# Kernel tuning notes

Measured on AMD Instinct MI355X. Metric: run time of the kernel, lower is better.

Reference implementation:

```python
import jax, jax.numpy as jnp
import numpy as np
from jax import lax

T = 8  # primary_vec_length


def setup_inputs() -> dict:
    key = jax.random.key(0)
    k1, k2, k3 = jax.random.split(key, 3)
    x = jax.random.normal(k1, (32, 256, 64, 64), dtype=jnp.float32)
    # Conv2d weight [out_ch, in_ch, kH, kW], kaiming-ish scale
    W = jax.random.normal(k2, (32, 256, 9, 9), dtype=jnp.float32) * 0.01
    b = jax.random.normal(k3, (32,), dtype=jnp.float32) * 0.01
    return {"x": x, "W": W, "b": b}


def reference(x, W, b):
    B = x.shape[0]
    # Conv2d(kernel=9, stride=2, valid). The original applies this conv T times
    # to identical stacked copies of x; compute it once and broadcast (same math).
    conv = lax.conv_general_dilated(
        x, W, window_strides=(2, 2), padding="VALID",
        dimension_numbers=("NCHW", "OIHW", "NCHW"))
    conv = conv + b[None, :, None, None]            # [B, C, H', W']
    s = jnp.broadcast_to(conv[:, None], (B, T) + conv.shape[1:])  # [B, T, C, H', W']
    # squash along dim=1 (the capsule-vector / time dim)
    sq = jnp.sum(s * s, axis=1, keepdims=True)      # [B, 1, C, H', W']
    scale = sq / (1.0 + sq) / jnp.sqrt(sq + 1e-8)
    squ = s * scale                                  # [B, T, C, H', W']
    squ = squ.reshape(B, T, -1)                      # [B, T, C*H'*W']
    squ = jnp.transpose(squ, (0, 2, 1))[..., None]   # [B, N, T, 1]
    return squ
```

## Files before the change

### kernel.cpp

```cpp
#include <hip/hip_runtime.h>
#include <hip/hip_bf16.h>
#include <stdint.h>

typedef _Float16 f16;
typedef _Float16 f16x8 __attribute__((ext_vector_type(8)));
typedef float f32x16 __attribute__((ext_vector_type(16)));
typedef float f32x4 __attribute__((ext_vector_type(4)));
typedef uint32_t u32x4 __attribute__((ext_vector_type(4)));
typedef uint32_t u32x2 __attribute__((ext_vector_type(2)));

#define MFMA(A, B, C) __builtin_amdgcn_mfma_f32_32x32x16_f16((A), (B), (C), 0, 0, 0)

__global__ __launch_bounds__(256) void nchw_to_nhwc_f16(
    const float* __restrict__ x, f16* __restrict__ xt) {
  __shared__ __align__(16) uint32_t tile[64 * 128];
  const int bh = blockIdx.x;
  const int t = threadIdx.x;
  const float* src = x + (size_t)(bh >> 6) * (256 * 4096) + (bh & 63) * 64;

  const int w4 = t & 15;
  const int cq = t >> 4;
  const int xorv = 4 * (w4 & 7);
#pragma unroll
  for (int it = 0; it < 4; ++it) {
    const int c0 = it * 64 + cq * 4;
    float4 v0 = *(const float4*)(src + (size_t)(c0 + 0) * 4096 + w4 * 4);
    float4 v1 = *(const float4*)(src + (size_t)(c0 + 1) * 4096 + w4 * 4);
    float4 v2 = *(const float4*)(src + (size_t)(c0 + 2) * 4096 + w4 * 4);
    float4 v3 = *(const float4*)(src + (size_t)(c0 + 3) * 4096 + w4 * 4);
    const float* p0 = (const float*)&v0;
    const float* p1 = (const float*)&v1;
    const float* p2 = (const float*)&v2;
    const float* p3 = (const float*)&v3;
    const int u = it * 32 + cq * 2;
#pragma unroll
    for (int jw = 0; jw < 4; ++jw) {
      f16 h0 = (f16)p0[jw], h1 = (f16)p1[jw], h2 = (f16)p2[jw], h3 = (f16)p3[jw];
      uint32_t lo = (uint32_t)__builtin_bit_cast(uint16_t, h0) |
                    ((uint32_t)__builtin_bit_cast(uint16_t, h1) << 16);
      uint32_t hi = (uint32_t)__builtin_bit_cast(uint16_t, h2) |
                    ((uint32_t)__builtin_bit_cast(uint16_t, h3) << 16);
      u32x2 pk = {lo, hi};
      const int w = w4 * 4 + jw;
      *(u32x2*)&tile[w * 128 + (u ^ xorv)] = pk;
    }
  }
  __syncthreads();
  f16* dstb = xt + (size_t)bh * 16384;
#pragma unroll
  for (int it = 0; it < 8; ++it) {
    const int n = it * 256 + t;
    const int w2 = n & 31;
    const int par = (n >> 5) & 1;
    const int g8 = n >> 6;
    const int w = par + 2 * w2;
    const u32x4 v = *(const u32x4*)&tile[w * 128 + ((g8 * 4) ^ (4 * ((w >> 2) & 7)))];
    *(u32x4*)(dstb + n * 8) = v;
  }
}

__global__ __launch_bounds__(256) void pack_w(const float* __restrict__ W,
                                              f16* __restrict__ wt) {
  __shared__ float lds[10368];
  const int t = threadIdx.x;
  const int co = blockIdx.x >> 1;
  const int cih = blockIdx.x & 1;
  const float* src = W + (size_t)(co * 256 + cih * 128) * 81;
  for (int i = t; i < 10368; i += 256) lds[i] = src[i];
  __syncthreads();
  for (int j = t; j < 1296; j += 256) {
    const int kk = j >> 4;
    const int t16 = j & 15;
    const int cicl = t16 >> 2;
    const int sg = t16 & 3;
    const int cin = ((sg >> 1) & 1) * 16 + (sg & 1) * 8;
    f16 tmp[8];
#pragma unroll
    for (int e = 0; e < 8; ++e)
      tmp[e] = (f16)lds[(cicl * 32 + cin + e) * 81 + kk];
    const int cic = cih * 4 + cicl;
    *(f16x8*)&wt[(size_t)(((kk * 8 + cic) * 4 + sg) * 32 + co) * 8] = *(f16x8*)tmp;
  }
}

__global__ __launch_bounds__(256, 3) void conv_direct(
    const f16* __restrict__ xt, const f16* __restrict__ wt,
    float* __restrict__ convp) {
  __shared__ float red[4 * 32 * 33];
  const int tid = threadIdx.x;
  const int lane = tid & 63;
  const int wave = tid >> 6;
  const int m = lane & 31;
  const int hh = lane >> 5;

  const int blk = blockIdx.x;
  const int xcd = blk & 7;
  const int r = blk >> 3;
  const int i4 = r / 28;
  const int rr = r - i4 * 28;
  const int bimg = xcd * 4 + i4;
  const int ohp = rr >> 1;
  const int cih = rr & 1;
  const int cic = cih * 4 + wave;

  const char* xb = (const char*)xt;
  const char* wb = (const char*)wt;

  const char* ab = xb + ((size_t)(bimg * 64 + 4 * ohp) * 32768 +
                         cic * 4096 + hh * 1024 + m * 16);
  const int boff = cic * 2048 + hh * 512 + m * 16;

#define ALOAD(AB, KW, P) \
  (*(const f16x8*)((AB) + (P) * 2048 + ((KW)&1) * 512 + ((KW) >> 1) * 16))
#define BLOAD(KK, S) \
  (*(const f16x8*)(wb + (size_t)(KK) * 16384 + (S) * 1024 + boff))

  f32x16 acc0, acc1;
#pragma unroll
  for (int i = 0; i < 16; ++i) { acc0[i] = 0.f; acc1[i] = 0.f; }

#define SLAB_BODY(T0A, T1A, KKB0, KKB1)                                        \
  {                                                                            \
    f16x8 a0[3], a1[3], b00[3], b01[3], b10[3], b11[3];                        \
    _Pragma("unroll") for (int k = 0; k < 3; ++k) {                            \
      a0[k] = ALOAD(ab, k, 0);                                                 \
      a1[k] = ALOAD(ab, k, 1);                                                 \
      if (T0A) { b00[k] = BLOAD((KKB0) + k, 0); b01[k] = BLOAD((KKB0) + k, 1); } \
      if (T1A) { b10[k] = BLOAD((KKB1) + k, 0); b11[k] = BLOAD((KKB1) + k, 1); } \
    }                                                                          \
    _Pragma("unroll") for (int kw = 0; kw < 9; ++kw) {                         \
      const int sl = kw % 3;                                                   \
      const f16x8 ca0 = a0[sl], ca1 = a1[sl];                                  \
      f16x8 t00, t01, t10, t11;                                                \
      if (T0A) { t00 = b00[sl]; t01 = b01[sl]; }                               \
      if (T1A) { t10 = b10[sl]; t11 = b11[sl]; }                               \
      if (kw + 3 < 9) {                                                        \
        a0[sl] = ALOAD(ab, kw + 3, 0);                                         \
        a1[sl] = ALOAD(ab, kw + 3, 1);                                         \
        if (T0A) { b00[sl] = BLOAD((KKB0) + kw + 3, 0);                        \
                   b01[sl] = BLOAD((KKB0) + kw + 3, 1); }                      \
        if (T1A) { b10[sl] = BLOAD((KKB1) + kw + 3, 0);                        \
                   b11[sl] = BLOAD((KKB1) + kw + 3, 1); }                      \
      }                                                                        \
      if (T0A) { acc0 = MFMA(ca0, t00, acc0); acc0 = MFMA(ca1, t01, acc0); }   \
      if (T1A) { acc1 = MFMA(ca0, t10, acc1); acc1 = MFMA(ca1, t11, acc1); }   \
    }                                                                          \
  }

  for (int j = 0; j < 2; ++j) {
    SLAB_BODY(1, 0, j * 9, 0)
    ab += 32768;
  }
  for (int j = 2; j < 9; ++j) {
    SLAB_BODY(1, 1, j * 9, (j - 2) * 9)
    ab += 32768;
  }
  for (int j = 9; j < 11; ++j) {
    SLAB_BODY(0, 1, 0, (j - 2) * 9)
    ab += 32768;
  }
#undef SLAB_BODY
#undef ALOAD
#undef BLOAD

  const int mm = tid >> 3;
  const int c0 = (tid & 7) * 4;
#pragma unroll
  for (int half = 0; half < 2; ++half) {
    __syncthreads();
#pragma unroll
    for (int rI = 0; rI < 16; ++rI) {
      const int row = (rI & 3) + 8 * (rI >> 2) + 4 * hh;
      red[(wave * 32 + row) * 33 + m] = half ? acc1[rI] : acc0[rI];
    }
    __syncthreads();
    if (mm < 28) {
      float s0 = 0.f, s1 = 0.f, s2 = 0.f, s3 = 0.f;
#pragma unroll
      for (int w = 0; w < 4; ++w) {
        const float* rp = red + (w * 32 + mm) * 33 + c0;
        s0 += rp[0]; s1 += rp[1]; s2 += rp[2]; s3 += rp[3];
      }
      const f32x4 o4 = {s0, s1, s2, s3};
      const int p = bimg * 784 + (2 * ohp + half) * 28 + mm;
      *(f32x4*)&convp[(size_t)cih * 802816 + (size_t)p * 32 + c0] = o4;
    }
  }
}

__global__ __launch_bounds__(256) void epilogue(const float* __restrict__ convp,
                                                const float* __restrict__ bias,
                                                float* __restrict__ out) {
  const int gi = blockIdx.x * 256 + threadIdx.x;
  const int base = gi * 8;
  const int p = gi >> 2;
  const int co0 = (gi & 3) * 8;
  const int bi = p / 784;
  const int pix = p - bi * 784;
  f32x4 v0 = {0.f, 0.f, 0.f, 0.f}, v1 = {0.f, 0.f, 0.f, 0.f};
#pragma unroll
  for (int qq = 0; qq < 2; ++qq) {
    v0 += *(const f32x4*)&convp[(size_t)qq * 802816 + base];
    v1 += *(const f32x4*)&convp[(size_t)qq * 802816 + base + 4];
  }
  float vb[8];
#pragma unroll
  for (int jj = 0; jj < 4; ++jj) {
    vb[jj] = v0[jj] + bias[co0 + jj];
    vb[4 + jj] = v1[jj] + bias[co0 + 4 + jj];
  }
  float* ob = out + (size_t)bi * 200704 + pix * 8;
#pragma unroll
  for (int jj = 0; jj < 8; ++jj) {
    const float vv = vb[jj];
    const float sq = 8.f * vv * vv;
    const float scale = sq / ((1.f + sq) * sqrtf(sq + 1e-8f));
    const float y = vv * scale;
    const f32x4 qv = {y, y, y, y};
    float* o = ob + (size_t)(co0 + jj) * 6272;
    *(f32x4*)o = qv;
    *(f32x4*)(o + 4) = qv;
  }
}

extern "C" void kernel_launch(void* const* d_in, const int* in_sizes, int n_in,
                              void* d_out, int out_size, void* d_ws,
                              size_t ws_size, hipStream_t stream) {
  const float* x = (const float*)d_in[0];
  const float* W = (const float*)d_in[1];
  const float* bias = (const float*)d_in[2];
  float* out = (float*)d_out;

  char* ws = (char*)d_ws;
  f16* xt = (f16*)ws;
  f16* wt = (f16*)(ws + 67108864);
  float* convp = (float*)(ws + 67108864 + 1327104);

  nchw_to_nhwc_f16<<<dim3(2048), dim3(256), 0, stream>>>(x, xt);
  pack_w<<<dim3(64), dim3(256), 0, stream>>>(W, wt);
  conv_direct<<<dim3(896), dim3(256), 0, stream>>>(xt, wt, convp);
  epilogue<<<dim3(392), dim3(256), 0, stream>>>(convp, bias, out);
}
```

Baseline: 296.1 us.

## Stage conv weights into LDS with async global_load_lds double buffering

Each wave used to load the weight fragments for every kernel position straight from global memory into registers. Now the whole block cooperatively stages those fragments into a 32 KB shared-memory double buffer with global_load_lds, fetching the next position's weights while it computes the current one. Input fragments are still loaded from global memory one step ahead. This removes redundant per-wave weight traffic and frees registers, but adds a __syncthreads on every kernel step and more LDS per block, which may limit occupancy.

```diff
diff --git a/kernel.cpp b/kernel.cpp
--- a/kernel.cpp
+++ b/kernel.cpp
@@ -86,7 +86,7 @@
 __global__ __launch_bounds__(256, 3) void conv_direct(
     const f16* __restrict__ xt, const f16* __restrict__ wt,
     float* __restrict__ convp) {
-  __shared__ float red[4 * 32 * 33];
+  __shared__ __align__(16) char smem[32768];
   const int tid = threadIdx.x;
   const int lane = tid & 63;
   const int wave = tid >> 6;
@@ -108,61 +108,83 @@
 
   const char* ab = xb + ((size_t)(bimg * 64 + 4 * ohp) * 32768 +
                          cic * 4096 + hh * 1024 + m * 16);
-  const int boff = cic * 2048 + hh * 512 + m * 16;
+  const size_t cih8192 = (size_t)cih * 8192;
+  const int t16 = tid * 16;
+  char* stg = smem;
+  const int fragoff = wave * 2048 + hh * 512 + m * 16;
+
+#define GLDS(G, L)                                                            \
+  __builtin_amdgcn_global_load_lds(                                           \
+      (const __attribute__((address_space(1))) void*)(G),                     \
+      (__attribute__((address_space(3))) void*)(L), 16, 0, 0)
 
 #define ALOAD(AB, KW, P) \
-  (*(const f16x8*)((AB) + (P) * 2048 + ((KW)&1) * 512 + ((KW) >> 1) * 16))
-#define BLOAD(KK, S) \
-  (*(const f16x8*)(wb + (size_t)(KK) * 16384 + (S) * 1024 + boff))
+  (*(const f16x8*)((AB) + (P)*2048 + ((KW)&1) * 512 + ((KW) >> 1) * 16))
+
+#define STAGE(DST, KKA, KKB)                                                  \
+  {                                                                           \
+    const char* sA = wb + (size_t)(KKA)*16384 + cih8192 + t16;                \
+    const char* sB = wb + (size_t)(KKB)*16384 + cih8192 + t16;                \
+    char* d = (DST) + t16;                                                    \
+    GLDS(sA, d);                                                              \
+    GLDS(sA + 4096, d + 4096);                                                \
+    GLDS(sB, d + 8192);                                                       \
+    GLDS(sB + 4096, d + 12288);                                               \
+  }
 
   f32x16 acc0, acc1;
 #pragma unroll
   for (int i = 0; i < 16; ++i) { acc0[i] = 0.f; acc1[i] = 0.f; }
 
-#define SLAB_BODY(T0A, T1A, KKB0, KKB1)                                        \
-  {                                                                            \
-    f16x8 a0[3], a1[3], b00[3], b01[3], b10[3], b11[3];                        \
-    _Pragma("unroll") for (int k = 0; k < 3; ++k) {                            \
-      a0[k] = ALOAD(ab, k, 0);                                                 \
-      a1[k] = ALOAD(ab, k, 1);                                                 \
-      if (T0A) { b00[k] = BLOAD((KKB0) + k, 0); b01[k] = BLOAD((KKB0) + k, 1); } \
-      if (T1A) { b10[k] = BLOAD((KKB1) + k, 0); b11[k] = BLOAD((KKB1) + k, 1); } \
-    }                                                                          \
-    _Pragma("unroll") for (int kw = 0; kw < 9; ++kw) {                         \
-      const int sl = kw % 3;                                                   \
-      const f16x8 ca0 = a0[sl], ca1 = a1[sl];                                  \
-      f16x8 t00, t01, t10, t11;                                                \
-      if (T0A) { t00 = b00[sl]; t01 = b01[sl]; }                               \
-      if (T1A) { t10 = b10[sl]; t11 = b11[sl]; }                               \
-      if (kw + 3 < 9) {                                                        \
-        a0[sl] = ALOAD(ab, kw + 3, 0);                                         \
-        a1[sl] = ALOAD(ab, kw + 3, 1);                                         \
-        if (T0A) { b00[sl] = BLOAD((KKB0) + kw + 3, 0);                        \
-                   b01[sl] = BLOAD((KKB0) + kw + 3, 1); }                      \
-        if (T1A) { b10[sl] = BLOAD((KKB1) + kw + 3, 0);                        \
-                   b11[sl] = BLOAD((KKB1) + kw + 3, 1); }                      \
-      }                                                                        \
-      if (T0A) { acc0 = MFMA(ca0, t00, acc0); acc0 = MFMA(ca1, t01, acc0); }   \
-      if (T1A) { acc1 = MFMA(ca0, t10, acc1); acc1 = MFMA(ca1, t11, acc1); }   \
-    }                                                                          \
-  }
-
-  for (int j = 0; j < 2; ++j) {
-    SLAB_BODY(1, 0, j * 9, 0)
-    ab += 32768;
-  }
-  for (int j = 2; j < 9; ++j) {
-    SLAB_BODY(1, 1, j * 9, (j - 2) * 9)
-    ab += 32768;
-  }
-  for (int j = 9; j < 11; ++j) {
-    SLAB_BODY(0, 1, 0, (j - 2) * 9)
-    ab += 32768;
-  }
-#undef SLAB_BODY
+  STAGE(stg, 0, 0)
+  f16x8 a0n = ALOAD(ab, 0, 0), a1n = ALOAD(ab, 0, 1);
+  int p = 0;
+
+#define STEP(T0A, T1A, NKKA, NKKB, ABN, NKW, LAST)                            \
+  {                                                                           \
+    __syncthreads();                                                          \
+    if (!(LAST)) STAGE(stg + (p ^ 1) * 16384, NKKA, NKKB)                     \
+    const f16x8 ca0 = a0n, ca1 = a1n;                                         \
+    if (!(LAST)) { a0n = ALOAD(ABN, NKW, 0); a1n = ALOAD(ABN, NKW, 1); }      \
+    const char* bp = stg + p * 16384 + fragoff;                               \
+    if (T0A) {                                                                \
+      acc0 = MFMA(ca0, *(const f16x8*)(bp), acc0);                            \
+      acc0 = MFMA(ca1, *(const f16x8*)(bp + 1024), acc0);                     \
+    }                                                                         \
+    if (T1A) {                                                                \
+      acc1 = MFMA(ca0, *(const f16x8*)(bp + 8192), acc1);                     \
+      acc1 = MFMA(ca1, *(const f16x8*)(bp + 9216), acc1);                     \
+    }                                                                         \
+    p ^= 1;                                                                   \
+  }
+
+#define SLAB9(T0A, T1A, KKA0, KKB0, NSA, NSB, ISLAST)                         \
+  {                                                                           \
+    _Pragma("unroll") for (int kw = 0; kw < 9; ++kw) {                        \
+      const int nkka = kw < 8 ? (KKA0) + kw + 1 : (NSA);                      \
+      const int nkkb = kw < 8 ? (KKB0) + kw + 1 : (NSB);                      \
+      const char* abn = kw < 8 ? ab : ab + 32768;                             \
+      const int nkw = kw < 8 ? kw + 1 : 0;                                    \
+      STEP(T0A, T1A, nkka, nkkb, abn, nkw, (ISLAST) && kw == 8)               \
+    }                                                                         \
+    ab += 32768;                                                              \
+  }
+
+  SLAB9(1, 0, 0, 0, 9, 0, 0)
+  SLAB9(1, 0, 9, 0, 18, 0, 0)
+  for (int j = 2; j < 8; ++j) {
+    SLAB9(1, 1, j * 9, (j - 2) * 9, (j + 1) * 9, (j - 1) * 9, 0)
+  }
+  SLAB9(1, 1, 72, 54, 0, 63, 0)
+  SLAB9(0, 1, 0, 63, 0, 72, 0)
+  SLAB9(0, 1, 0, 72, 0, 0, 1)
+#undef SLAB9
+#undef STEP
+#undef STAGE
 #undef ALOAD
-#undef BLOAD
-
+#undef GLDS
+
+  float* red = (float*)smem;
   const int mm = tid >> 3;
   const int c0 = (tid & 7) * 4;
 #pragma unroll
@@ -182,8 +204,8 @@
         s0 += rp[0]; s1 += rp[1]; s2 += rp[2]; s3 += rp[3];
       }
       const f32x4 o4 = {s0, s1, s2, s3};
-      const int p = bimg * 784 + (2 * ohp + half) * 28 + mm;
-      *(f32x4*)&convp[(size_t)cih * 802816 + (size_t)p * 32 + c0] = o4;
+      const int pp = bimg * 784 + (2 * ohp + half) * 28 + mm;
+      *(f32x4*)&convp[(size_t)cih * 802816 + (size_t)pp * 32 + c0] = o4;
     }
   }
 }
```

Result: slower. 376.9 us (+27.3%).

## Compute four output rows per block, reusing weight fragments across rows

Applied to the files above, without the earlier changes.

Each conv block now produces four output rows instead of two, halving the grid. Loops are reordered so kw and kernel-row parity are outer, and each weight fragment loaded once feeds four accumulators. Input rows are shifted through registers in a sliding window. This cuts redundant weight loads per MFMA at the cost of more registers, lower occupancy (launch bound 2) and fewer blocks to spread across CUs.

```diff
diff --git a/kernel.cpp b/kernel.cpp
--- a/kernel.cpp
+++ b/kernel.cpp
@@ -83,7 +83,7 @@
   }
 }
 
-__global__ __launch_bounds__(256, 3) void conv_direct(
+__global__ __launch_bounds__(256, 2) void conv_direct(
     const f16* __restrict__ xt, const f16* __restrict__ wt,
     float* __restrict__ convp) {
   __shared__ float red[4 * 32 * 33];
@@ -96,96 +96,98 @@
   const int blk = blockIdx.x;
   const int xcd = blk & 7;
   const int r = blk >> 3;
-  const int i4 = r / 28;
-  const int rr = r - i4 * 28;
+  const int i4 = r / 14;
+  const int rr = r - i4 * 14;
   const int bimg = xcd * 4 + i4;
-  const int ohp = rr >> 1;
+  const int og = rr >> 1;
   const int cih = rr & 1;
   const int cic = cih * 4 + wave;
 
   const char* xb = (const char*)xt;
   const char* wb = (const char*)wt;
 
-  const char* ab = xb + ((size_t)(bimg * 64 + 4 * ohp) * 32768 +
-                         cic * 4096 + hh * 1024 + m * 16);
+  const char* base = xb + ((size_t)(bimg * 64 + 8 * og) * 32768 +
+                           cic * 4096 + hh * 1024 + m * 16);
   const int boff = cic * 2048 + hh * 512 + m * 16;
 
-#define ALOAD(AB, KW, P) \
-  (*(const f16x8*)((AB) + (P) * 2048 + ((KW)&1) * 512 + ((KW) >> 1) * 16))
-#define BLOAD(KK, S) \
+#define ALOADR(H, KW, P)                                                 \
+  (*(const f16x8*)(base + (size_t)(H) * 32768 + (P) * 2048 +             \
+                   ((KW) & 1) * 512 + ((KW) >> 1) * 16))
+#define BLOADK(KK, S) \
   (*(const f16x8*)(wb + (size_t)(KK) * 16384 + (S) * 1024 + boff))
 
-  f32x16 acc0, acc1;
-#pragma unroll
-  for (int i = 0; i < 16; ++i) { acc0[i] = 0.f; acc1[i] = 0.f; }
-
-#define SLAB_BODY(T0A, T1A, KKB0, KKB1)                                        \
-  {                                                                            \
-    f16x8 a0[3], a1[3], b00[3], b01[3], b10[3], b11[3];                        \
-    _Pragma("unroll") for (int k = 0; k < 3; ++k) {                            \
-      a0[k] = ALOAD(ab, k, 0);                                                 \
-      a1[k] = ALOAD(ab, k, 1);                                                 \
-      if (T0A) { b00[k] = BLOAD((KKB0) + k, 0); b01[k] = BLOAD((KKB0) + k, 1); } \
-      if (T1A) { b10[k] = BLOAD((KKB1) + k, 0); b11[k] = BLOAD((KKB1) + k, 1); } \
-    }                                                                          \
-    _Pragma("unroll") for (int kw = 0; kw < 9; ++kw) {                         \
-      const int sl = kw % 3;                                                   \
-      const f16x8 ca0 = a0[sl], ca1 = a1[sl];                                  \
-      f16x8 t00, t01, t10, t11;                                                \
-      if (T0A) { t00 = b00[sl]; t01 = b01[sl]; }                               \
-      if (T1A) { t10 = b10[sl]; t11 = b11[sl]; }                               \
-      if (kw + 3 < 9) {                                                        \
-        a0[sl] = ALOAD(ab, kw + 3, 0);                                         \
-        a1[sl] = ALOAD(ab, kw + 3, 1);                                         \
-        if (T0A) { b00[sl] = BLOAD((KKB0) + kw + 3, 0);                        \
-                   b01[sl] = BLOAD((KKB0) + kw + 3, 1); }                      \
-        if (T1A) { b10[sl] = BLOAD((KKB1) + kw + 3, 0);                        \
-                   b11[sl] = BLOAD((KKB1) + kw + 3, 1); }                      \
-      }                                                                        \
-      if (T0A) { acc0 = MFMA(ca0, t00, acc0); acc0 = MFMA(ca1, t01, acc0); }   \
-      if (T1A) { acc1 = MFMA(ca0, t10, acc1); acc1 = MFMA(ca1, t11, acc1); }   \
-    }                                                                          \
-  }
-
-  for (int j = 0; j < 2; ++j) {
-    SLAB_BODY(1, 0, j * 9, 0)
-    ab += 32768;
-  }
-  for (int j = 2; j < 9; ++j) {
-    SLAB_BODY(1, 1, j * 9, (j - 2) * 9)
-    ab += 32768;
-  }
-  for (int j = 9; j < 11; ++j) {
-    SLAB_BODY(0, 1, 0, (j - 2) * 9)
-    ab += 32768;
-  }
-#undef SLAB_BODY
-#undef ALOAD
-#undef BLOAD
+  f32x16 acc0, acc1, acc2, acc3;
+#pragma unroll
+  for (int i = 0; i < 16; ++i) {
+    acc0[i] = 0.f; acc1[i] = 0.f; acc2[i] = 0.f; acc3[i] = 0.f;
+  }
+
+#pragma unroll
+  for (int kw = 0; kw < 9; ++kw) {
+#pragma unroll
+    for (int par = 0; par < 2; ++par) {
+      const int nk = par ? 4 : 5;
+      f16x8 bb0[5], bb1[5];
+#pragma unroll
+      for (int i = 0; i < 5; ++i) {
+        if (i < nk) {
+          bb0[i] = BLOADK((par + 2 * i) * 9 + kw, 0);
+          bb1[i] = BLOADK((par + 2 * i) * 9 + kw, 1);
+        }
+      }
+      f16x8 a00 = ALOADR(par + 0, kw, 0), a01 = ALOADR(par + 0, kw, 1);
+      f16x8 a10 = ALOADR(par + 2, kw, 0), a11 = ALOADR(par + 2, kw, 1);
+      f16x8 a20 = ALOADR(par + 4, kw, 0), a21 = ALOADR(par + 4, kw, 1);
+      f16x8 a30 = ALOADR(par + 6, kw, 0), a31 = ALOADR(par + 6, kw, 1);
+#pragma unroll
+      for (int i = 0; i < nk; ++i) {
+        f16x8 n0, n1;
+        if (i + 1 < nk) {
+          n0 = ALOADR(par + 2 * i + 8, kw, 0);
+          n1 = ALOADR(par + 2 * i + 8, kw, 1);
+        }
+        acc0 = MFMA(a00, bb0[i], acc0); acc0 = MFMA(a01, bb1[i], acc0);
+        acc1 = MFMA(a10, bb0[i], acc1); acc1 = MFMA(a11, bb1[i], acc1);
+        acc2 = MFMA(a20, bb0[i], acc2); acc2 = MFMA(a21, bb1[i], acc2);
+        acc3 = MFMA(a30, bb0[i], acc3); acc3 = MFMA(a31, bb1[i], acc3);
+        if (i + 1 < nk) {
+          a00 = a10; a01 = a11;
+          a10 = a20; a11 = a21;
+          a20 = a30; a21 = a31;
+          a30 = n0;  a31 = n1;
+        }
+      }
+    }
+  }
+#undef ALOADR
+#undef BLOADK
 
   const int mm = tid >> 3;
   const int c0 = (tid & 7) * 4;
-#pragma unroll
-  for (int half = 0; half < 2; ++half) {
-    __syncthreads();
-#pragma unroll
-    for (int rI = 0; rI < 16; ++rI) {
-      const int row = (rI & 3) + 8 * (rI >> 2) + 4 * hh;
-      red[(wave * 32 + row) * 33 + m] = half ? acc1[rI] : acc0[rI];
-    }
-    __syncthreads();
-    if (mm < 28) {
-      float s0 = 0.f, s1 = 0.f, s2 = 0.f, s3 = 0.f;
-#pragma unroll
-      for (int w = 0; w < 4; ++w) {
-        const float* rp = red + (w * 32 + mm) * 33 + c0;
-        s0 += rp[0]; s1 += rp[1]; s2 += rp[2]; s3 += rp[3];
-      }
-      const f32x4 o4 = {s0, s1, s2, s3};
-      const int p = bimg * 784 + (2 * ohp + half) * 28 + mm;
-      *(f32x4*)&convp[(size_t)cih * 802816 + (size_t)p * 32 + c0] = o4;
-    }
-  }
+#define REDUCE_ROUND(ACC, T)                                                   \
+  {                                                                            \
+    __syncthreads();                                                           \
+    _Pragma("unroll") for (int rI = 0; rI < 16; ++rI) {                        \
+      const int row = (rI & 3) + 8 * (rI >> 2) + 4 * hh;                       \
+      red[(wave * 32 + row) * 33 + m] = (ACC)[rI];                             \
+    }                                                                          \
+    __syncthreads();                                                           \
+    if (mm < 28) {                                                             \
+      float s0 = 0.f, s1 = 0.f, s2 = 0.f, s3 = 0.f;                            \
+      _Pragma("unroll") for (int w = 0; w < 4; ++w) {                          \
+        const float* rp = red + (w * 32 + mm) * 33 + c0;                       \
+        s0 += rp[0]; s1 += rp[1]; s2 += rp[2]; s3 += rp[3];                    \
+      }                                                                        \
+      const f32x4 o4 = {s0, s1, s2, s3};                                       \
+      const int p = bimg * 784 + (4 * og + (T)) * 28 + mm;                     \
+      *(f32x4*)&convp[(size_t)cih * 802816 + (size_t)p * 32 + c0] = o4;        \
+    }                                                                          \
+  }
+  REDUCE_ROUND(acc0, 0)
+  REDUCE_ROUND(acc1, 1)
+  REDUCE_ROUND(acc2, 2)
+  REDUCE_ROUND(acc3, 3)
+#undef REDUCE_ROUND
 }
 
 __global__ __launch_bounds__(256) void epilogue(const float* __restrict__ convp,
@@ -238,6 +240,6 @@
 
   nchw_to_nhwc_f16<<<dim3(2048), dim3(256), 0, stream>>>(x, xt);
   pack_w<<<dim3(64), dim3(256), 0, stream>>>(W, wt);
-  conv_direct<<<dim3(896), dim3(256), 0, stream>>>(xt, wt, convp);
+  conv_direct<<<dim3(448), dim3(256), 0, stream>>>(xt, wt, convp);
   epilogue<<<dim3(392), dim3(256), 0, stream>>>(convp, bias, out);
 }
```

Result: slower. 312.6 us (+5.6%).

## Share staged weights in LDS across output-row waves, split input channels across blocks

Applied to the files above, without the earlier changes.

Restructures the conv work split so each block owns one input-channel chunk and four waves cover different output row pairs. The weight slab for each kh is staged into a 4-deep LDS ring via global_load_lds and shared by all waves, replacing per-wave direct global weight loads. The cross-wave LDS reduction is removed: each wave writes its partial directly, which grows the partial buffer to 8 channel chunks that the epilogue now sums. The costs are more partial-sum traffic in the epilogue, some idle waves (ohp>=14), lower occupancy, and a barrier per slab.

```diff
diff --git a/kernel.cpp b/kernel.cpp
--- a/kernel.cpp
+++ b/kernel.cpp
@@ -83,10 +83,10 @@
   }
 }
 
-__global__ __launch_bounds__(256, 3) void conv_direct(
+__global__ __launch_bounds__(256, 2) void conv_direct(
     const f16* __restrict__ xt, const f16* __restrict__ wt,
     float* __restrict__ convp) {
-  __shared__ float red[4 * 32 * 33];
+  __shared__ __align__(16) char stg[4 * 18432];
   const int tid = threadIdx.x;
   const int lane = tid & 63;
   const int wave = tid >> 6;
@@ -96,94 +96,102 @@
   const int blk = blockIdx.x;
   const int xcd = blk & 7;
   const int r = blk >> 3;
-  const int i4 = r / 28;
-  const int rr = r - i4 * 28;
+  const int i4 = r >> 5;
+  const int rr = r & 31;
+  const int og = rr >> 3;
+  const int cic = rr & 7;
   const int bimg = xcd * 4 + i4;
-  const int ohp = rr >> 1;
-  const int cih = rr & 1;
-  const int cic = cih * 4 + wave;
+  const int ohp = og * 4 + wave;
+  const bool active = (ohp < 14);
 
   const char* xb = (const char*)xt;
   const char* wb = (const char*)wt;
 
   const char* ab = xb + ((size_t)(bimg * 64 + 4 * ohp) * 32768 +
                          cic * 4096 + hh * 1024 + m * 16);
-  const int boff = cic * 2048 + hh * 512 + m * 16;
+  const size_t cic2048 = (size_t)cic * 2048;
+  const int fragoff = hh * 512 + m * 16;
+
+#define GLDS(G, L)                                                            \
+  __builtin_amdgcn_global_load_lds(                                           \
+      (const __attribute__((address_space(1))) void*)(G),                     \
+      (__attribute__((address_space(3))) void*)(L), 16, 0, 0)
 
 #define ALOAD(AB, KW, P) \
-  (*(const f16x8*)((AB) + (P) * 2048 + ((KW)&1) * 512 + ((KW) >> 1) * 16))
-#define BLOAD(KK, S) \
-  (*(const f16x8*)(wb + (size_t)(KK) * 16384 + (S) * 1024 + boff))
+  (*(const f16x8*)((AB) + (P) * 2048 + ((KW) & 1) * 512 + ((KW) >> 1) * 16))
+#define LDSF(P) (*(const f16x8*)(P))
+
+#define STAGE(JN)                                                             \
+  {                                                                           \
+    const int kkb = (JN) * 9;                                                 \
+    char* db = stg + ((JN) & 3) * 18432;                                      \
+    _Pragma("unroll") for (int i = 0; i < 4; ++i) {                           \
+      const int u = tid + 256 * i;                                            \
+      GLDS(wb + (size_t)(kkb + (u >> 7)) * 16384 + cic2048 + (u & 127) * 16,  \
+           db + u * 16);                                                      \
+    }                                                                         \
+    if (tid < 128) {                                                          \
+      GLDS(wb + (size_t)(kkb + 8) * 16384 + cic2048 + tid * 16,               \
+           db + 16384 + tid * 16);                                            \
+    }                                                                         \
+  }
 
   f32x16 acc0, acc1;
 #pragma unroll
   for (int i = 0; i < 16; ++i) { acc0[i] = 0.f; acc1[i] = 0.f; }
 
-#define SLAB_BODY(T0A, T1A, KKB0, KKB1)                                        \
-  {                                                                            \
-    f16x8 a0[3], a1[3], b00[3], b01[3], b10[3], b11[3];                        \
-    _Pragma("unroll") for (int k = 0; k < 3; ++k) {                            \
-      a0[k] = ALOAD(ab, k, 0);                                                 \
-      a1[k] = ALOAD(ab, k, 1);                                                 \
-      if (T0A) { b00[k] = BLOAD((KKB0) + k, 0); b01[k] = BLOAD((KKB0) + k, 1); } \
-      if (T1A) { b10[k] = BLOAD((KKB1) + k, 0); b11[k] = BLOAD((KKB1) + k, 1); } \
-    }                                                                          \
-    _Pragma("unroll") for (int kw = 0; kw < 9; ++kw) {                         \
-      const int sl = kw % 3;                                                   \
-      const f16x8 ca0 = a0[sl], ca1 = a1[sl];                                  \
-      f16x8 t00, t01, t10, t11;                                                \
-      if (T0A) { t00 = b00[sl]; t01 = b01[sl]; }                               \
-      if (T1A) { t10 = b10[sl]; t11 = b11[sl]; }                               \
-      if (kw + 3 < 9) {                                                        \
-        a0[sl] = ALOAD(ab, kw + 3, 0);                                         \
-        a1[sl] = ALOAD(ab, kw + 3, 1);                                         \
-        if (T0A) { b00[sl] = BLOAD((KKB0) + kw + 3, 0);                        \
-                   b01[sl] = BLOAD((KKB0) + kw + 3, 1); }                      \
-        if (T1A) { b10[sl] = BLOAD((KKB1) + kw + 3, 0);                        \
-                   b11[sl] = BLOAD((KKB1) + kw + 3, 1); }                      \
-      }                                                                        \
-      if (T0A) { acc0 = MFMA(ca0, t00, acc0); acc0 = MFMA(ca1, t01, acc0); }   \
-      if (T1A) { acc1 = MFMA(ca0, t10, acc1); acc1 = MFMA(ca1, t11, acc1); }   \
-    }                                                                          \
-  }
-
-  for (int j = 0; j < 2; ++j) {
-    SLAB_BODY(1, 0, j * 9, 0)
+  STAGE(0)
+
+  for (int j = 0; j < 11; ++j) {
+    __syncthreads();
+    if (j < 8) STAGE(j + 1)
+    if (active) {
+      const char* s0 = stg + (j & 3) * 18432 + fragoff;
+      const char* s1 = stg + ((j + 2) & 3) * 18432 + fragoff;
+      if (j >= 2 && j <= 8) {
+#pragma unroll
+        for (int kw = 0; kw < 9; ++kw) {
+          const f16x8 a0 = ALOAD(ab, kw, 0), a1 = ALOAD(ab, kw, 1);
+          acc0 = MFMA(a0, LDSF(s0 + kw * 2048), acc0);
+          acc0 = MFMA(a1, LDSF(s0 + kw * 2048 + 1024), acc0);
+          acc1 = MFMA(a0, LDSF(s1 + kw * 2048), acc1);
+          acc1 = MFMA(a1, LDSF(s1 + kw * 2048 + 1024), acc1);
+        }
+      } else if (j < 2) {
+#pragma unroll
+        for (int kw = 0; kw < 9; ++kw) {
+          const f16x8 a0 = ALOAD(ab, kw, 0), a1 = ALOAD(ab, kw, 1);
+          acc0 = MFMA(a0, LDSF(s0 + kw * 2048), acc0);
+          acc0 = MFMA(a1, LDSF(s0 + kw * 2048 + 1024), acc0);
+        }
+      } else {
+#pragma unroll
+        for (int kw = 0; kw < 9; ++kw) {
+          const f16x8 a0 = ALOAD(ab, kw, 0), a1 = ALOAD(ab, kw, 1);
+          acc1 = MFMA(a0, LDSF(s1 + kw * 2048), acc1);
+          acc1 = MFMA(a1, LDSF(s1 + kw * 2048 + 1024), acc1);
+        }
+      }
+    }
     ab += 32768;
   }
-  for (int j = 2; j < 9; ++j) {
-    SLAB_BODY(1, 1, j * 9, (j - 2) * 9)
-    ab += 32768;
-  }
-  for (int j = 9; j < 11; ++j) {
-    SLAB_BODY(0, 1, 0, (j - 2) * 9)
-    ab += 32768;
-  }
-#undef SLAB_BODY
+#undef STAGE
 #undef ALOAD
-#undef BLOAD
-
-  const int mm = tid >> 3;
-  const int c0 = (tid & 7) * 4;
-#pragma unroll
-  for (int half = 0; half < 2; ++half) {
-    __syncthreads();
-#pragma unroll
-    for (int rI = 0; rI < 16; ++rI) {
-      const int row = (rI & 3) + 8 * (rI >> 2) + 4 * hh;
-      red[(wave * 32 + row) * 33 + m] = half ? acc1[rI] : acc0[rI];
-    }
-    __syncthreads();
-    if (mm < 28) {
-      float s0 = 0.f, s1 = 0.f, s2 = 0.f, s3 = 0.f;
-#pragma unroll
-      for (int w = 0; w < 4; ++w) {
-        const float* rp = red + (w * 32 + mm) * 33 + c0;
-        s0 += rp[0]; s1 += rp[1]; s2 += rp[2]; s3 += rp[3];
+#undef LDSF
+#undef GLDS
+
+  if (active) {
+#pragma unroll
+    for (int tile = 0; tile < 2; ++tile) {
+      const int oh = 2 * ohp + tile;
+      float* cp = convp + (size_t)cic * 802816 +
+                  ((size_t)bimg * 784 + oh * 28) * 32 + m;
+      const f32x16& a = tile ? acc1 : acc0;
+#pragma unroll
+      for (int rI = 0; rI < 16; ++rI) {
+        const int ow = (rI & 3) + 8 * (rI >> 2) + 4 * hh;
+        if (ow < 28) cp[ow * 32] = a[rI];
       }
-      const f32x4 o4 = {s0, s1, s2, s3};
-      const int p = bimg * 784 + (2 * ohp + half) * 28 + mm;
-      *(f32x4*)&convp[(size_t)cih * 802816 + (size_t)p * 32 + c0] = o4;
     }
   }
 }
@@ -199,7 +207,7 @@
   const int pix = p - bi * 784;
   f32x4 v0 = {0.f, 0.f, 0.f, 0.f}, v1 = {0.f, 0.f, 0.f, 0.f};
 #pragma unroll
-  for (int qq = 0; qq < 2; ++qq) {
+  for (int qq = 0; qq < 8; ++qq) {
     v0 += *(const f32x4*)&convp[(size_t)qq * 802816 + base];
     v1 += *(const f32x4*)&convp[(size_t)qq * 802816 + base + 4];
   }
@@ -238,6 +246,6 @@
 
   nchw_to_nhwc_f16<<<dim3(2048), dim3(256), 0, stream>>>(x, xt);
   pack_w<<<dim3(64), dim3(256), 0, stream>>>(W, wt);
-  conv_direct<<<dim3(896), dim3(256), 0, stream>>>(xt, wt, convp);
+  conv_direct<<<dim3(1024), dim3(256), 0, stream>>>(xt, wt, convp);
   epilogue<<<dim3(392), dim3(256), 0, stream>>>(convp, bias, out);
 }
```

Measured after the change: 285.5 us. -3.6%, faster.
